# Kernel optimization log

Measured on AMD Instinct MI355X. Metric: run time of the kernel, lower is better.

The kernel has to match this reference:

```python
import jax, jax.numpy as jnp
import numpy as np

D_MODEL = 1024
NUM_HEADS = 16
DEPTH = D_MODEL // NUM_HEADS
B, S = 2, 2048
NEG = -1e9


def setup_inputs() -> dict:
    key = jax.random.key(0)
    ks = jax.random.split(key, 12)
    sc = 1.0 / np.sqrt(D_MODEL)
    inp = {
        "query": jax.random.normal(ks[0], (B, S, D_MODEL), jnp.float32),
        "key_in": jax.random.normal(ks[1], (B, S, D_MODEL), jnp.float32),
        "value": jax.random.normal(ks[2], (B, S, D_MODEL), jnp.float32),
        # causal mask: 1.0 where attention is disallowed (upper triangle)
        "mask": (1.0 - jnp.tril(jnp.ones((S, S), jnp.float32)))[None, None, :, :],
        "wq": jax.random.normal(ks[3], (D_MODEL, D_MODEL), jnp.float32) * sc,
        "bq": jnp.zeros((D_MODEL,), jnp.float32),
        "wk": jax.random.normal(ks[4], (D_MODEL, D_MODEL), jnp.float32) * sc,
        "bk": jnp.zeros((D_MODEL,), jnp.float32),
        "wv": jax.random.normal(ks[5], (D_MODEL, D_MODEL), jnp.float32) * sc,
        "bv": jnp.zeros((D_MODEL,), jnp.float32),
        "wo": jax.random.normal(ks[6], (D_MODEL, D_MODEL), jnp.float32) * sc,
        "bo": jnp.zeros((D_MODEL,), jnp.float32),
    }
    return inp


def _split_heads(x):
    # [B,S,D] -> [B,H,S,depth]
    b, s, _ = x.shape
    return x.reshape(b, s, NUM_HEADS, DEPTH).transpose(0, 2, 1, 3)


def reference(query, key_in, value, mask, wq, bq, wk, bk, wv, bv, wo, bo):
    q = _split_heads(query @ wq + bq)
    k = _split_heads(key_in @ wk + bk)
    v = _split_heads(value @ wv + bv)
    scale = 1.0 / jnp.sqrt(jnp.asarray(DEPTH, jnp.float32))
    logits = jnp.einsum("bhqd,bhkd->bhqk", q, k) * scale + mask * NEG
    attn = jax.nn.softmax(logits, axis=-1)
    out = jnp.einsum("bhqk,bhkd->bhqd", attn, v)  # [B,H,S,depth]
    out = out.transpose(0, 2, 1, 3).reshape(query.shape[0], -1, D_MODEL)
    return out @ wo + bo
```

## Files before the change

### kernel.cpp

```cpp
#include <hip/hip_runtime.h>
#include <hip/hip_bf16.h>
#include <cstdint>
#include <cstddef>

#define D_MODEL 1024
#define NHEADS  16
#define DEPTH   64
#define BATCH   2
#define SEQ     2048
#define M_TOT   (BATCH*SEQ)
#define QK_SCALE 0.18033688011112042f

typedef __attribute__((ext_vector_type(8)))  __bf16 bf16x8;
typedef __attribute__((ext_vector_type(4)))  float  f32x4;
typedef __attribute__((ext_vector_type(16))) float  f32x16;

__device__ inline unsigned short f2bf(float f){
  unsigned u = __float_as_uint(f);
  u += 0x7FFFu + ((u>>16)&1u);
  return (unsigned short)(u>>16);
}
__device__ inline unsigned cvtpk(float lo, float hi){
  unsigned r;
  asm("v_cvt_pk_bf16_f32 %0, %1, %2" : "=v"(r) : "v"(lo), "v"(hi));
  return r;
}
__device__ inline float fexp2(float x){
  float r;
  asm("v_exp_f32 %0, %1" : "=v"(r) : "v"(x));
  return r;
}
__device__ inline int bswap23(int x){
  return (x & ~12) | ((x & 4) << 1) | ((x & 8) >> 1);
}

#define AS1(p) ((__attribute__((address_space(1))) void*)(p))
#define AS3(p) ((__attribute__((address_space(3))) void*)(p))

__global__ void cvt3(const float* __restrict__ q, const float* __restrict__ k,
                     const float* __restrict__ v,
                     unsigned short* oq, unsigned short* ok, unsigned short* ov, int n4){
  const float* in = blockIdx.z==0 ? q : blockIdx.z==1 ? k : v;
  unsigned short* out = blockIdx.z==0 ? oq : blockIdx.z==1 ? ok : ov;
  int i = blockIdx.x*blockDim.x + threadIdx.x;
  if (i >= n4) return;
  float4 val = ((const float4*)in)[i];
  ushort4 o;
  o.x = f2bf(val.x); o.y = f2bf(val.y); o.z = f2bf(val.z); o.w = f2bf(val.w);
  ((ushort4*)out)[i] = o;
}

__global__ void tcvt4(const float* __restrict__ w0, const float* __restrict__ w1,
                      const float* __restrict__ w2, const float* __restrict__ w3,
                      unsigned short* o0, unsigned short* o1,
                      unsigned short* o2, unsigned short* o3){
  const float* W = blockIdx.z==0 ? w0 : blockIdx.z==1 ? w1 : blockIdx.z==2 ? w2 : w3;
  unsigned short* Wt = blockIdx.z==0 ? o0 : blockIdx.z==1 ? o1 : blockIdx.z==2 ? o2 : o3;
  const bool perm = (blockIdx.z == 3);
  __shared__ float t[32][33];
  int bx = blockIdx.x*32, by = blockIdx.y*32;
  for (int j = threadIdx.y; j < 32; j += 8)
    t[j][threadIdx.x] = W[(size_t)(by+j)*D_MODEL + bx + threadIdx.x];
  __syncthreads();
  for (int j = threadIdx.y; j < 32; j += 8){
    int col = by + threadIdx.x;
    if (perm) col = bswap23(col);
    Wt[(size_t)(bx+j)*D_MODEL + col] = f2bf(t[threadIdx.x][j]);
  }
}

#define BM 128
#define BN 128
#define BK 64
#define GK 1024

#define STAGE_TILE(lds, P, RSB, k0, ROWS) \
  _Pragma("unroll") \
  for (int i2=0; i2<(ROWS)/32; i2++){ \
    int x = i2*4096 + tid*16; \
    int row_ = x >> 7; \
    int cb_ = (x & 127) ^ ((row_&7)<<4); \
    __builtin_amdgcn_global_load_lds( \
      AS1((P) + (size_t)row_*(RSB) + (k0)*2 + cb_), \
      AS3((char*)(lds) + x), 16, 0, 0); \
  }

#define FRAG(lds, row_, kk) \
  (*(const bf16x8*)((const char*)(lds) + (row_)*128 + \
     (((kk)*64 + (lane>>4)*16) ^ (((row_)&7)<<4))))

__global__ __launch_bounds__(256) void gemm_qkv(
    const unsigned short* __restrict__ Xq, const unsigned short* __restrict__ Xk,
    const unsigned short* __restrict__ Xv,
    const unsigned short* __restrict__ Wq, const unsigned short* __restrict__ Wk,
    const unsigned short* __restrict__ Wv,
    const float* __restrict__ bq, const float* __restrict__ bk, const float* __restrict__ bv,
    unsigned short* Qh, unsigned short* Kh, unsigned short* Vth)
{
  __shared__ __align__(16) short As[BM*BK];
  __shared__ __align__(16) short Bs[BN*BK];
  const int z = blockIdx.z;
  const unsigned short* A  = z==0 ? Xq : z==1 ? Xk : Xv;
  const unsigned short* Bt = z==0 ? Wq : z==1 ? Wk : Wv;
  const float* bias        = z==0 ? bq : z==1 ? bk : bv;

  const int tid = threadIdx.x, lane = tid & 63, wave = tid >> 6;
  const int m0 = blockIdx.x*BM, n0 = blockIdx.y*BN;
  const int wm = wave >> 1, wn = wave & 1;

  f32x4 acc[4][4];
  #pragma unroll
  for (int i=0;i<4;i++)
    #pragma unroll
    for (int j=0;j<4;j++)
      acc[i][j] = (f32x4){0.f,0.f,0.f,0.f};

  const char* Abase = (const char*)A + (size_t)m0*GK*2;
  const char* Bbase = (const char*)Bt + (size_t)n0*GK*2;

  for (int k0 = 0; k0 < GK; k0 += BK){
    STAGE_TILE(As, Abase, GK*2, k0, BM)
    STAGE_TILE(Bs, Bbase, GK*2, k0, BN)
    __syncthreads();
    #pragma unroll
    for (int kk=0;kk<2;kk++){
      bf16x8 af[4], bfv[4];
      #pragma unroll
      for (int i=0;i<4;i++)
        af[i] = FRAG(As, wm*64 + i*16 + (lane&15), kk);
      #pragma unroll
      for (int j=0;j<4;j++)
        bfv[j] = FRAG(Bs, wn*64 + j*16 + (lane&15), kk);
      #pragma unroll
      for (int i=0;i<4;i++)
        #pragma unroll
        for (int j=0;j<4;j++)
          acc[i][j] = __builtin_amdgcn_mfma_f32_16x16x32_bf16(af[i], bfv[j], acc[i][j], 0,0,0);
    }
    __syncthreads();
  }

  #pragma unroll
  for (int i=0;i<4;i++)
    #pragma unroll
    for (int j=0;j<4;j++)
      #pragma unroll
      for (int r=0;r<4;r++){
        int gr = m0 + wm*64 + i*16 + (lane>>4)*4 + r;
        int gc = n0 + wn*64 + j*16 + (lane&15);
        float v = acc[i][j][r] + bias[gc];
        int b = gr>>11, s = gr&2047, h = gc>>6, d = gc&63;
        if (z == 0){
          v *= QK_SCALE;
          Qh[(((size_t)(b*NHEADS+h))*SEQ + s)*DEPTH + d] = f2bf(v);
        } else if (z == 1){
          Kh[(((size_t)(b*NHEADS+h))*SEQ + s)*DEPTH + d] = f2bf(v);
        } else {
          int sp = bswap23(s);
          Vth[(((size_t)(b*NHEADS+h))*DEPTH + d)*SEQ + sp] = f2bf(v);
        }
      }
}

#define BM2 64
__global__ __launch_bounds__(256) void gemm_out(
    const unsigned short* __restrict__ A,
    const unsigned short* __restrict__ Bt,
    const float* __restrict__ bias,
    float* __restrict__ Cout)
{
  __shared__ __align__(16) short As[BM2*BK];
  __shared__ __align__(16) short Bs[BN*BK];
  const int tid = threadIdx.x, lane = tid & 63, wave = tid >> 6;
  const int m0 = blockIdx.x*BM2, n0 = blockIdx.y*BN;
  const int wm = wave >> 1, wn = wave & 1;

  f32x4 acc[2][4];
  #pragma unroll
  for (int i=0;i<2;i++)
    #pragma unroll
    for (int j=0;j<4;j++)
      acc[i][j] = (f32x4){0.f,0.f,0.f,0.f};

  const char* Abase = (const char*)A + (size_t)m0*GK*2;
  const char* Bbase = (const char*)Bt + (size_t)n0*GK*2;

  for (int k0 = 0; k0 < GK; k0 += BK){
    STAGE_TILE(As, Abase, GK*2, k0, BM2)
    STAGE_TILE(Bs, Bbase, GK*2, k0, BN)
    __syncthreads();
    #pragma unroll
    for (int kk=0;kk<2;kk++){
      bf16x8 af[2], bfv[4];
      #pragma unroll
      for (int i=0;i<2;i++)
        af[i] = FRAG(As, wm*32 + i*16 + (lane&15), kk);
      #pragma unroll
      for (int j=0;j<4;j++)
        bfv[j] = FRAG(Bs, wn*64 + j*16 + (lane&15), kk);
      #pragma unroll
      for (int i=0;i<2;i++)
        #pragma unroll
        for (int j=0;j<4;j++)
          acc[i][j] = __builtin_amdgcn_mfma_f32_16x16x32_bf16(af[i], bfv[j], acc[i][j], 0,0,0);
    }
    __syncthreads();
  }

  #pragma unroll
  for (int i=0;i<2;i++)
    #pragma unroll
    for (int j=0;j<4;j++)
      #pragma unroll
      for (int r=0;r<4;r++){
        int gr = m0 + wm*32 + i*16 + (lane>>4)*4 + r;
        int gc = n0 + wn*64 + j*16 + (lane&15);
        Cout[(size_t)gr*D_MODEL + gc] = acc[i][j][r] + bias[gc];
      }
}

__global__ __launch_bounds__(512,4) void attn_fwd(
  const unsigned short* __restrict__ Qh,
  const unsigned short* __restrict__ Kh,
  const unsigned short* __restrict__ Vt,
  unsigned short* __restrict__ AO)
{
  __shared__ __align__(16) short Ks[2][4096];
  __shared__ __align__(16) short Vs[2][4096];
  __shared__ float cbS[2][128];

  const int tid = threadIdx.x, lane = tid & 63, w = tid >> 6;
  const int h = lane >> 5, ql = lane & 31;
  const int qh = w & 1, kh = (w >> 1) & 1, tl = w >> 2;
  const int pj = blockIdx.x, bh = blockIdx.y;
  const size_t hb = (size_t)bh * SEQ * DEPTH;
  const char* Kb = (const char*)(Kh + hb);
  const char* Vb = (const char*)(Vt + hb);
  const unsigned short* Qb = Qh + hb;
  const int bb = bh >> 4, hd = bh & 15;
  const int swz = (ql & 7) << 4;

  auto STAGE = [&](int buf, int t){
    const int kv0 = t*64;
    #pragma unroll
    for (int i=0;i<2;i++){
      int c = (w&3)*2 + i;
      int x = c*1024 + lane*16;
      int row = x >> 7;
      int cb = (x & 127) ^ ((row&7)<<4);
      if (w < 4)
        __builtin_amdgcn_global_load_lds(
          AS1(Kb + (size_t)(kv0+row)*128 + cb),
          AS3((char*)&Ks[buf][0] + c*1024), 16, 0, 0);
      else
        __builtin_amdgcn_global_load_lds(
          AS1(Vb + ((size_t)row*SEQ + kv0)*2 + cb),
          AS3((char*)&Vs[buf][0] + c*1024), 16, 0, 0);
    }
  };

  const int jtw = tl ? pj : (31 - pj);
  const int Q0 = jtw*64 + qh*32;
  const int qmax = Q0 + 31;
  const int Tblock = 32 - pj;

  bf16x8 qreg[4];
  {
    const unsigned short* qp = Qb + (size_t)(Q0 + ql)*DEPTH + h*8;
    #pragma unroll
    for (int c=0;c<4;c++) qreg[c] = *(const bf16x8*)(qp + c*16);
  }

  f32x16 oacc[2];
  #pragma unroll
  for (int dh=0;dh<2;dh++)
    #pragma unroll
    for (int r=0;r<16;r++) oacc[dh][r] = 0.f;
  float s = 0.f;

  STAGE(0, 0);
  __syncthreads();
  int cur = 0;

  #pragma unroll 1
  for (int t = 0; t < Tblock; ++t){
    if (t+1 < Tblock) STAGE(cur^1, t+1);
    const int kvb = t*64 + kh*32;

    if (kvb <= qmax){
      f32x16 sa;
      #pragma unroll
      for (int r=0;r<16;r++) sa[r] = -16.0f;
      #pragma unroll
      for (int c=0;c<4;c++){
        bf16x8 kf = *(const bf16x8*)((const char*)&Ks[cur][0]
                      + (kh*32 + ql)*128 + ((32*c + 16*h) ^ swz));
        sa = __builtin_amdgcn_mfma_f32_32x32x16_bf16(kf, qreg[c], sa, 0,0,0);
      }

      if (kvb + 31 > Q0){
        const int qg = Q0 + ql - kvb;
        #pragma unroll
        for (int r=0;r<16;r++){
          int pos = (r&3) + 8*(r>>2) + 4*h;
          sa[r] = (pos > qg) ? -1e9f : sa[r];
        }
      }

      float s0=0.f, s1=0.f, s2=0.f, s3=0.f;
      #pragma unroll
      for (int r=0;r<16;r++){
        float p = fexp2(sa[r]);
        sa[r] = p;
        if ((r&3)==0) s0 += p; else if ((r&3)==1) s1 += p;
        else if ((r&3)==2) s2 += p; else s3 += p;
      }
      s += (s0+s1)+(s2+s3);

      bf16x8 pw[2];
      #pragma unroll
      for (int ks=0;ks<2;ks++){
        const int mm = 8*ks;
        union { unsigned u[4]; bf16x8 v; } pk;
        pk.u[0] = cvtpk(sa[mm+0], sa[mm+1]);
        pk.u[1] = cvtpk(sa[mm+2], sa[mm+3]);
        pk.u[2] = cvtpk(sa[mm+4], sa[mm+5]);
        pk.u[3] = cvtpk(sa[mm+6], sa[mm+7]);
        pw[ks] = pk.v;
      }

      #pragma unroll
      for (int ks=0;ks<2;ks++){
        #pragma unroll
        for (int dh=0;dh<2;dh++){
          bf16x8 vf = *(const bf16x8*)((const char*)&Vs[cur][0]
                        + (dh*32 + ql)*128 + ((kh*64 + ks*32 + 16*h) ^ swz));
          oacc[dh] = __builtin_amdgcn_mfma_f32_32x32x16_bf16(vf, pw[ks], oacc[dh], 0,0,0);
        }
      }
    }

    __syncthreads();
    cur ^= 1;
  }

  float* cbO  = (tl == 0) ? (float*)&Ks[0][0] : (float*)&Vs[0][0];
  float* cbSp = &cbS[tl][0];
  if (kh == 1){
    #pragma unroll
    for (int dh=0;dh<2;dh++)
      #pragma unroll
      for (int r=0;r<16;r++)
        cbO[(dh*16+r)*128 + qh*64 + lane] = oacc[dh][r];
    cbSp[qh*64 + lane] = s;
  }
  __syncthreads();
  if (kh == 0){
    #pragma unroll
    for (int dh=0;dh<2;dh++)
      #pragma unroll
      for (int r=0;r<16;r++)
        oacc[dh][r] += cbO[(dh*16+r)*128 + qh*64 + lane];
    s += cbSp[qh*64 + lane];
    float st = s + __shfl_xor(s, 32, 64);
    float inv = 1.0f / st;
    #pragma unroll
    for (int dh=0;dh<2;dh++)
      #pragma unroll
      for (int r=0;r<16;r++) oacc[dh][r] *= inv;

    unsigned short* orow = AO + ((size_t)bb*SEQ + (Q0 + ql))*D_MODEL + hd*DEPTH;
    #pragma unroll
    for (int dh=0;dh<2;dh++)
      #pragma unroll
      for (int g=0; g<2; g++){
        uint4 st4;
        st4.x = cvtpk(oacc[dh][8*g+0], oacc[dh][8*g+1]);
        st4.y = cvtpk(oacc[dh][8*g+2], oacc[dh][8*g+3]);
        st4.z = cvtpk(oacc[dh][8*g+4], oacc[dh][8*g+5]);
        st4.w = cvtpk(oacc[dh][8*g+6], oacc[dh][8*g+7]);
        *(uint4*)(orow + dh*32 + g*16 + h*8) = st4;
      }
  }
}

extern "C" void kernel_launch(void* const* d_in, const int* in_sizes, int n_in,
                              void* d_out, int out_size, void* d_ws, size_t ws_size,
                              hipStream_t stream) {
  const float* query  = (const float*)d_in[0];
  const float* key_in = (const float*)d_in[1];
  const float* value  = (const float*)d_in[2];
  const float* wq = (const float*)d_in[4];
  const float* bq = (const float*)d_in[5];
  const float* wk = (const float*)d_in[6];
  const float* bk = (const float*)d_in[7];
  const float* wv = (const float*)d_in[8];
  const float* bv = (const float*)d_in[9];
  const float* wo = (const float*)d_in[10];
  const float* bo = (const float*)d_in[11];

  char* ws = (char*)d_ws;
  const size_t MB = 1u<<20;
  unsigned short* Xq  = (unsigned short*)(ws + 0*MB);
  unsigned short* Xk  = (unsigned short*)(ws + 8*MB);
  unsigned short* Xv  = (unsigned short*)(ws + 16*MB);
  unsigned short* Wtq = (unsigned short*)(ws + 24*MB);
  unsigned short* Wtk = (unsigned short*)(ws + 26*MB);
  unsigned short* Wtv = (unsigned short*)(ws + 28*MB);
  unsigned short* Wto = (unsigned short*)(ws + 30*MB);
  unsigned short* Qh  = (unsigned short*)(ws + 32*MB);
  unsigned short* Kh  = (unsigned short*)(ws + 40*MB);
  unsigned short* Vth = (unsigned short*)(ws + 48*MB);
  unsigned short* AO  = (unsigned short*)(ws + 56*MB);

  const int n4 = (M_TOT*D_MODEL)/4;
  cvt3<<<dim3(n4/256,1,3), 256, 0, stream>>>(query, key_in, value, Xq, Xk, Xv, n4);
  tcvt4<<<dim3(32,32,4), dim3(32,8), 0, stream>>>(wq, wk, wv, wo, Wtq, Wtk, Wtv, Wto);

  gemm_qkv<<<dim3(M_TOT/BM, D_MODEL/BN, 3), 256, 0, stream>>>(
      Xq, Xk, Xv, Wtq, Wtk, Wtv, bq, bk, bv, Qh, Kh, Vth);

  attn_fwd<<<dim3(16, BATCH*NHEADS), 512, 0, stream>>>(Qh, Kh, Vth, AO);

  gemm_out<<<dim3(M_TOT/BM2, D_MODEL/BN), 256, 0, stream>>>(AO, Wto, bo, (float*)d_out);
}
```

Before: 118.8 us.

## Fuse fp32-to-bf16 input conversion into QKV GEMM with register prefetch

Removes the separate cvt3 kernel and has gemm_qkv read fp32 activations directly. Each tile is converted to bf16 in registers and stored to LDS, with the next K-slice prefetched into registers. This saves a kernel launch and a full write/read round trip of the bf16 activations. BK is halved to 32, the LDS XOR swizzle is dropped (risking bank conflicts), and launch bounds request 2 blocks per CU; gemm_out is changed to the same BK and layout.

```diff
diff --git a/kernel.cpp b/kernel.cpp
--- a/kernel.cpp
+++ b/kernel.cpp
@@ -36,19 +36,6 @@
 
 #define AS1(p) ((__attribute__((address_space(1))) void*)(p))
 #define AS3(p) ((__attribute__((address_space(3))) void*)(p))
-
-__global__ void cvt3(const float* __restrict__ q, const float* __restrict__ k,
-                     const float* __restrict__ v,
-                     unsigned short* oq, unsigned short* ok, unsigned short* ov, int n4){
-  const float* in = blockIdx.z==0 ? q : blockIdx.z==1 ? k : v;
-  unsigned short* out = blockIdx.z==0 ? oq : blockIdx.z==1 ? ok : ov;
-  int i = blockIdx.x*blockDim.x + threadIdx.x;
-  if (i >= n4) return;
-  float4 val = ((const float4*)in)[i];
-  ushort4 o;
-  o.x = f2bf(val.x); o.y = f2bf(val.y); o.z = f2bf(val.z); o.w = f2bf(val.w);
-  ((ushort4*)out)[i] = o;
-}
 
 __global__ void tcvt4(const float* __restrict__ w0, const float* __restrict__ w1,
                       const float* __restrict__ w2, const float* __restrict__ w3,
@@ -71,27 +58,12 @@
 
 #define BM 128
 #define BN 128
-#define BK 64
+#define BK 32
 #define GK 1024
 
-#define STAGE_TILE(lds, P, RSB, k0, ROWS) \
-  _Pragma("unroll") \
-  for (int i2=0; i2<(ROWS)/32; i2++){ \
-    int x = i2*4096 + tid*16; \
-    int row_ = x >> 7; \
-    int cb_ = (x & 127) ^ ((row_&7)<<4); \
-    __builtin_amdgcn_global_load_lds( \
-      AS1((P) + (size_t)row_*(RSB) + (k0)*2 + cb_), \
-      AS3((char*)(lds) + x), 16, 0, 0); \
-  }
-
-#define FRAG(lds, row_, kk) \
-  (*(const bf16x8*)((const char*)(lds) + (row_)*128 + \
-     (((kk)*64 + (lane>>4)*16) ^ (((row_)&7)<<4))))
-
-__global__ __launch_bounds__(256) void gemm_qkv(
-    const unsigned short* __restrict__ Xq, const unsigned short* __restrict__ Xk,
-    const unsigned short* __restrict__ Xv,
+__global__ __launch_bounds__(256,2) void gemm_qkv(
+    const float* __restrict__ Xfq, const float* __restrict__ Xfk,
+    const float* __restrict__ Xfv,
     const unsigned short* __restrict__ Wq, const unsigned short* __restrict__ Wk,
     const unsigned short* __restrict__ Wv,
     const float* __restrict__ bq, const float* __restrict__ bk, const float* __restrict__ bv,
@@ -100,9 +72,9 @@
   __shared__ __align__(16) short As[BM*BK];
   __shared__ __align__(16) short Bs[BN*BK];
   const int z = blockIdx.z;
-  const unsigned short* A  = z==0 ? Xq : z==1 ? Xk : Xv;
-  const unsigned short* Bt = z==0 ? Wq : z==1 ? Wk : Wv;
-  const float* bias        = z==0 ? bq : z==1 ? bk : bv;
+  const float* Af          = z==0 ? Xfq : z==1 ? Xfk : Xfv;
+  const unsigned short* Bt = z==0 ? Wq  : z==1 ? Wk  : Wv;
+  const float* bias        = z==0 ? bq  : z==1 ? bk  : bv;
 
   const int tid = threadIdx.x, lane = tid & 63, wave = tid >> 6;
   const int m0 = blockIdx.x*BM, n0 = blockIdx.y*BN;
@@ -115,29 +87,55 @@
     for (int j=0;j<4;j++)
       acc[i][j] = (f32x4){0.f,0.f,0.f,0.f};
 
-  const char* Abase = (const char*)A + (size_t)m0*GK*2;
+  const char* Afb   = (const char*)Af + (size_t)m0*GK*4;
   const char* Bbase = (const char*)Bt + (size_t)n0*GK*2;
-
+  const int arow = tid >> 2;
+  const int acb  = (tid & 3) * 32;
+
+  float4 alo[2], ahi[2];
+  auto LOADA = [&](int k0){
+    #pragma unroll
+    for (int c=0;c<2;c++){
+      const char* p = Afb + (size_t)(c*64 + arow)*(GK*4) + k0*4 + acb;
+      alo[c] = *(const float4*)p;
+      ahi[c] = *(const float4*)(p + 16);
+    }
+  };
+
+  LOADA(0);
   for (int k0 = 0; k0 < GK; k0 += BK){
-    STAGE_TILE(As, Abase, GK*2, k0, BM)
-    STAGE_TILE(Bs, Bbase, GK*2, k0, BN)
-    __syncthreads();
-    #pragma unroll
-    for (int kk=0;kk<2;kk++){
-      bf16x8 af[4], bfv[4];
-      #pragma unroll
-      for (int i=0;i<4;i++)
-        af[i] = FRAG(As, wm*64 + i*16 + (lane&15), kk);
-      #pragma unroll
-      for (int j=0;j<4;j++)
-        bfv[j] = FRAG(Bs, wn*64 + j*16 + (lane&15), kk);
-      #pragma unroll
-      for (int i=0;i<4;i++)
-        #pragma unroll
-        for (int j=0;j<4;j++)
-          acc[i][j] = __builtin_amdgcn_mfma_f32_16x16x32_bf16(af[i], bfv[j], acc[i][j], 0,0,0);
+    uint4 pk[2];
+    #pragma unroll
+    for (int c=0;c<2;c++){
+      pk[c].x = cvtpk(alo[c].x, alo[c].y);
+      pk[c].y = cvtpk(alo[c].z, alo[c].w);
+      pk[c].z = cvtpk(ahi[c].x, ahi[c].y);
+      pk[c].w = cvtpk(ahi[c].z, ahi[c].w);
     }
     __syncthreads();
+    #pragma unroll
+    for (int c=0;c<2;c++)
+      *(uint4*)((char*)As + c*4096 + tid*16) = pk[c];
+    #pragma unroll
+    for (int c=0;c<2;c++)
+      __builtin_amdgcn_global_load_lds(
+        AS1(Bbase + (size_t)(c*64 + arow)*(GK*2) + k0*2 + (tid&3)*16),
+        AS3((char*)Bs + c*4096 + tid*16), 16, 0, 0);
+    __syncthreads();
+    if (k0 + BK < GK) LOADA(k0 + BK);
+
+    bf16x8 af[4], bfv[4];
+    #pragma unroll
+    for (int i=0;i<4;i++)
+      af[i] = *(const bf16x8*)((const char*)As + (wm*64 + i*16 + (lane&15))*64 + (lane>>4)*16);
+    #pragma unroll
+    for (int j=0;j<4;j++)
+      bfv[j] = *(const bf16x8*)((const char*)Bs + (wn*64 + j*16 + (lane&15))*64 + (lane>>4)*16);
+    #pragma unroll
+    for (int i=0;i<4;i++)
+      #pragma unroll
+      for (int j=0;j<4;j++)
+        acc[i][j] = __builtin_amdgcn_mfma_f32_16x16x32_bf16(af[i], bfv[j], acc[i][j], 0,0,0);
   }
 
   #pragma unroll
@@ -163,7 +161,7 @@
 }
 
 #define BM2 64
-__global__ __launch_bounds__(256) void gemm_out(
+__global__ __launch_bounds__(256,2) void gemm_out(
     const unsigned short* __restrict__ A,
     const unsigned short* __restrict__ Bt,
     const float* __restrict__ bias,
@@ -186,24 +184,27 @@
   const char* Bbase = (const char*)Bt + (size_t)n0*GK*2;
 
   for (int k0 = 0; k0 < GK; k0 += BK){
-    STAGE_TILE(As, Abase, GK*2, k0, BM2)
-    STAGE_TILE(Bs, Bbase, GK*2, k0, BN)
+    __builtin_amdgcn_global_load_lds(
+      AS1(Abase + (size_t)(tid>>2)*(GK*2) + k0*2 + (tid&3)*16),
+      AS3((char*)As + tid*16), 16, 0, 0);
+    #pragma unroll
+    for (int c=0;c<2;c++)
+      __builtin_amdgcn_global_load_lds(
+        AS1(Bbase + (size_t)(c*64 + (tid>>2))*(GK*2) + k0*2 + (tid&3)*16),
+        AS3((char*)Bs + c*4096 + tid*16), 16, 0, 0);
     __syncthreads();
-    #pragma unroll
-    for (int kk=0;kk<2;kk++){
-      bf16x8 af[2], bfv[4];
-      #pragma unroll
-      for (int i=0;i<2;i++)
-        af[i] = FRAG(As, wm*32 + i*16 + (lane&15), kk);
+    bf16x8 af[2], bfv[4];
+    #pragma unroll
+    for (int i=0;i<2;i++)
+      af[i] = *(const bf16x8*)((const char*)As + (wm*32 + i*16 + (lane&15))*64 + (lane>>4)*16);
+    #pragma unroll
+    for (int j=0;j<4;j++)
+      bfv[j] = *(const bf16x8*)((const char*)Bs + (wn*64 + j*16 + (lane&15))*64 + (lane>>4)*16);
+    #pragma unroll
+    for (int i=0;i<2;i++)
       #pragma unroll
       for (int j=0;j<4;j++)
-        bfv[j] = FRAG(Bs, wn*64 + j*16 + (lane&15), kk);
-      #pragma unroll
-      for (int i=0;i<2;i++)
-        #pragma unroll
-        for (int j=0;j<4;j++)
-          acc[i][j] = __builtin_amdgcn_mfma_f32_16x16x32_bf16(af[i], bfv[j], acc[i][j], 0,0,0);
-    }
+        acc[i][j] = __builtin_amdgcn_mfma_f32_16x16x32_bf16(af[i], bfv[j], acc[i][j], 0,0,0);
     __syncthreads();
   }
 
@@ -401,9 +402,6 @@
 
   char* ws = (char*)d_ws;
   const size_t MB = 1u<<20;
-  unsigned short* Xq  = (unsigned short*)(ws + 0*MB);
-  unsigned short* Xk  = (unsigned short*)(ws + 8*MB);
-  unsigned short* Xv  = (unsigned short*)(ws + 16*MB);
   unsigned short* Wtq = (unsigned short*)(ws + 24*MB);
   unsigned short* Wtk = (unsigned short*)(ws + 26*MB);
   unsigned short* Wtv = (unsigned short*)(ws + 28*MB);
@@ -413,12 +411,10 @@
   unsigned short* Vth = (unsigned short*)(ws + 48*MB);
   unsigned short* AO  = (unsigned short*)(ws + 56*MB);
 
-  const int n4 = (M_TOT*D_MODEL)/4;
-  cvt3<<<dim3(n4/256,1,3), 256, 0, stream>>>(query, key_in, value, Xq, Xk, Xv, n4);
   tcvt4<<<dim3(32,32,4), dim3(32,8), 0, stream>>>(wq, wk, wv, wo, Wtq, Wtk, Wtv, Wto);
 
   gemm_qkv<<<dim3(M_TOT/BM, D_MODEL/BN, 3), 256, 0, stream>>>(
-      Xq, Xk, Xv, Wtq, Wtk, Wtv, bq, bk, bv, Qh, Kh, Vth);
+      query, key_in, value, Wtq, Wtk, Wtv, bq, bk, bv, Qh, Kh, Vth);
 
   attn_fwd<<<dim3(16, BATCH*NHEADS), 512, 0, stream>>>(Qh, Kh, Vth, AO);
 
```

Result: faster. 105.6 us (-11.1%).
